# Performance work log

Hardware: AMD Instinct MI355X
Metric: run time of the kernel (lower is better)

Reference implementation:

```python
import jax, jax.numpy as jnp
import numpy as np

LN_EPS = 1e-5

def _layernorm(x, g, b):
    mu = x.mean(-1, keepdims=True)
    var = ((x - mu) ** 2).mean(-1, keepdims=True)
    return (x - mu) * jax.lax.rsqrt(var + LN_EPS) * g + b

def setup_inputs() -> dict:
    key = jax.random.key(0)
    ks = jax.random.split(key, 5)
    B, S, H, V = 1, 1024, 768, 50257
    return {
        "hidden_states": jax.random.normal(ks[0], (B, S, H), jnp.float32),
        "attention_mask": jnp.ones((B, S), jnp.int32),
        "alpha": jnp.float32(0.1),
        "ln_gamma": jnp.ones((H,), jnp.float32),
        "ln_beta": jnp.zeros((H,), jnp.float32),
        "W1": jax.random.normal(ks[1], (H, H), jnp.float32) * 0.02,
        "b1": jnp.zeros((H,), jnp.float32),
        "W2": jax.random.normal(ks[2], (H, H), jnp.float32) * 0.02,
        "b2": jnp.zeros((H,), jnp.float32),
        "lm_head_w": jax.random.normal(ks[3], (V, H), jnp.float32) * 0.02,
        "n_processors": 4,
        "k_steps": 4,
    }

def reference(hidden_states, attention_mask, alpha, ln_gamma, ln_beta,
              W1, b1, W2, b2, lm_head_w, n_processors, k_steps):
    P = int(n_processors)
    K = int(k_steps)
    mask = attention_mask.astype(hidden_states.dtype)[..., None]        # [B,S,1]
    # processor_states: [P,B,S,H] (all initialized to the same hidden state)
    states = jnp.broadcast_to(hidden_states[None], (P,) + hidden_states.shape)
    for _ in range(K):
        # eval mode: dropout=identity, no noise -> mutate == mask multiply
        mut = states * mask                                             # [P,B,S,H]
        if P > 1:
            # mean of other processors = (sum_all - self)/(P-1)
            observe = (mut.sum(0, keepdims=True) - mut) / (P - 1)
        else:
            observe = jnp.zeros_like(mut)
        merged = mut + alpha * observe
        normed = _layernorm(merged, ln_gamma, ln_beta)
        h = jax.nn.gelu(jnp.einsum('pbsh,ih->pbsi', normed, W1) + b1,
                        approximate=False)
        delta = jnp.einsum('pbsi,hi->pbsh', h, W2) + b2
        states = (mut + delta) * mask
    consensus = states.mean(0)                                          # [B,S,H]
    logits = jnp.einsum('bsh,vh->bsv', consensus, lm_head_w)            # [B,S,V]
    processor_logits = jnp.einsum('pbsh,vh->pbsv', states, lm_head_w)   # [P,B,S,V]
    return logits, processor_logits, states
```

## Files before the change

kernel.cpp:

```cpp
#include <hip/hip_runtime.h>
#include <hip/hip_bf16.h>
#include <math.h>

#define S_LEN 1024
#define HDIM  768
#define NPROC 4
#define VOCAB 50257
#define KSTEPS 4

typedef __attribute__((ext_vector_type(4))) float f32x4;
typedef __attribute__((ext_vector_type(8))) short bf16x8;
typedef __attribute__((ext_vector_type(4))) short short4v;

static __device__ __forceinline__ ushort f2bf(float f) {
  union { __hip_bfloat16 b; ushort u; } cv;
  cv.b = __float2bfloat16(f);
  return cv.u;
}

#define GLOAD16(gp, lp) __builtin_amdgcn_global_load_lds( \
    (const __attribute__((address_space(1))) unsigned int*)(gp), \
    (__attribute__((address_space(3))) unsigned int*)(lp), 16, 0, 0)

__global__ __launch_bounds__(256) void prep_weights(
    const float* __restrict__ lmw, const float* __restrict__ W1,
    const float* __restrict__ W2, ushort* __restrict__ lm_bf,
    ushort* __restrict__ w1_bf, ushort* __restrict__ w2_bf,
    const float* __restrict__ hidden, const int* __restrict__ mask,
    const float* __restrict__ alphap, const float* __restrict__ gamma,
    const float* __restrict__ beta, ushort* __restrict__ normed) {
  const int LM4 = VOCAB * HDIM / 4;
  const int W4  = HDIM * HDIM / 4;
  const int LMB = (LM4 + 255) / 256;
  const int WB  = (W4 + 255) / 256;
  const int bid = blockIdx.x;
  const int tid = threadIdx.x;
  __shared__ float rs_[4], rq_[4];
  if (bid < LMB + 2 * WB) {
    const float* in; ushort* out; int n4, i;
    if (bid < LMB)           { in = lmw; out = lm_bf; n4 = LM4; i = bid * 256 + tid; }
    else if (bid < LMB + WB) { in = W1;  out = w1_bf; n4 = W4;  i = (bid - LMB) * 256 + tid; }
    else                     { in = W2;  out = w2_bf; n4 = W4;  i = (bid - LMB - WB) * 256 + tid; }
    if (i >= n4) return;
    f32x4 v = ((const f32x4*)in)[i];
    short4v o;
#pragma unroll
    for (int j = 0; j < 4; j++) o[j] = (short)f2bf(v[j]);
    ((short4v*)out)[i] = o;
  } else {
    const int s = bid - (LMB + 2 * WB);
    const float mk = (float)mask[s];
    const float a1 = 1.0f + alphap[0];
    float merged[3];
    float lsum = 0.f, lsq = 0.f;
#pragma unroll
    for (int e = 0; e < 3; e++) {
      const int h = tid + e * 256;
      float mg = hidden[(size_t)s * HDIM + h] * mk * a1;
      merged[e] = mg;
      lsum += mg;
      lsq += mg * mg;
    }
#pragma unroll
    for (int off = 32; off > 0; off >>= 1) {
      lsum += __shfl_down(lsum, off, 64);
      lsq  += __shfl_down(lsq, off, 64);
    }
    const int wv = tid >> 6, ln = tid & 63;
    if (ln == 0) { rs_[wv] = lsum; rq_[wv] = lsq; }
    __syncthreads();
    const float ts = rs_[0] + rs_[1] + rs_[2] + rs_[3];
    const float tq = rq_[0] + rq_[1] + rq_[2] + rq_[3];
    const float mu = ts * (1.f / HDIM);
    const float var = tq * (1.f / HDIM) - mu * mu;
    const float rstd = rsqrtf(var + 1e-5f);
#pragma unroll
    for (int e = 0; e < 3; e++) {
      const int h = tid + e * 256;
      float nv = (merged[e] - mu) * rstd * gamma[h] + beta[h];
      normed[(size_t)s * HDIM + h] = f2bf(nv);
    }
  }
}

__global__ __launch_bounds__(256) void bcast_logits(
    const float* __restrict__ src, float* __restrict__ dst) {
  const size_t n4 = (size_t)S_LEN * VOCAB / 4;
  for (size_t i = (size_t)blockIdx.x * 256 + threadIdx.x; i < n4;
       i += (size_t)gridDim.x * 256) {
    f32x4 v = ((const f32x4*)src)[i];
#pragma unroll
    for (int p = 0; p < NPROC; p++)
      ((f32x4*)dst)[(size_t)p * n4 + i] = v;
  }
}

__global__ __launch_bounds__(256) void merge_ln_p1(
    const float* __restrict__ src, const int* __restrict__ mask,
    const float* __restrict__ alphap, const float* __restrict__ gamma,
    const float* __restrict__ beta, ushort* __restrict__ normed) {
  const int s = blockIdx.x;
  const int tid = threadIdx.x;
  const float mk = (float)mask[s];
  const float a1 = 1.0f + alphap[0];
  float merged[3];
  float lsum = 0.f, lsq = 0.f;
#pragma unroll
  for (int e = 0; e < 3; e++) {
    const int h = tid + e * 256;
    float mg = src[(size_t)s * HDIM + h] * mk * a1;
    merged[e] = mg;
    lsum += mg;
    lsq += mg * mg;
  }
#pragma unroll
  for (int off = 32; off > 0; off >>= 1) {
    lsum += __shfl_down(lsum, off, 64);
    lsq  += __shfl_down(lsq, off, 64);
  }
  __shared__ float rs_[4], rq_[4];
  const int wv = tid >> 6, ln = tid & 63;
  if (ln == 0) { rs_[wv] = lsum; rq_[wv] = lsq; }
  __syncthreads();
  const float ts = rs_[0] + rs_[1] + rs_[2] + rs_[3];
  const float tq = rq_[0] + rq_[1] + rq_[2] + rq_[3];
  const float mu = ts * (1.f / HDIM);
  const float var = tq * (1.f / HDIM) - mu * mu;
  const float rstd = rsqrtf(var + 1e-5f);
#pragma unroll
  for (int e = 0; e < 3; e++) {
    const int h = tid + e * 256;
    float nv = (merged[e] - mu) * rstd * gamma[h] + beta[h];
    normed[(size_t)s * HDIM + h] = f2bf(nv);
  }
}

template <int MODE>
__global__ __launch_bounds__(256, 4) void gemm_mlp(
    const ushort* __restrict__ A, const ushort* __restrict__ B,
    const float* __restrict__ bias, ushort* __restrict__ out_bf,
    const float* __restrict__ src, float* __restrict__ dst,
    float* __restrict__ states, const int* __restrict__ mask) {
  __shared__ __align__(16) ushort lsA[3][4096];
  __shared__ __align__(16) ushort lsB[3][2048];
  const int tid = threadIdx.x;
  const int bx = blockIdx.x;
  const int mt = bx & 7;
  const int nt = bx >> 3;
  const int wv = tid >> 6, lane = tid & 63;
  const int wm = wv >> 1, wn = wv & 1;
  const int g = lane >> 4, lr = lane & 15;

  f32x4 acc[4][2];
#pragma unroll
  for (int i = 0; i < 4; i++)
#pragma unroll
    for (int j = 0; j < 2; j++) acc[i][j] = (f32x4){0.f, 0.f, 0.f, 0.f};

  const int koff = (tid & 3) * 8;
  const int arow0 = mt * 128 + (tid >> 2);
  const ushort* gA0 = A + (size_t)arow0 * HDIM + koff;
  const ushort* gA1 = gA0 + (size_t)64 * HDIM;
  const ushort* gB0 = B + (size_t)(nt * 64 + (tid >> 2)) * HDIM + koff;
  const int dstl = (tid >> 2) * 32 + (tid & 3) * 8;

#define STAGE(kt, buf) do {                      \
    const int o_ = (kt) * 32;                    \
    GLOAD16(gA0 + o_, &lsA[buf][dstl]);          \
    GLOAD16(gA1 + o_, &lsA[buf][2048 + dstl]);   \
    GLOAD16(gB0 + o_, &lsB[buf][dstl]);          \
  } while (0)

  constexpr int NT = HDIM / 32;
  STAGE(0, 0);
  STAGE(1, 1);
  STAGE(2, 2);
  int cur = 0;
  for (int kt = 0; kt < NT; ++kt) {
    if (kt < NT - 2)      asm volatile("s_waitcnt vmcnt(6)" ::: "memory");
    else if (kt == NT - 2) asm volatile("s_waitcnt vmcnt(3)" ::: "memory");
    else                  asm volatile("s_waitcnt vmcnt(0)" ::: "memory");
    __builtin_amdgcn_s_barrier();
    __builtin_amdgcn_sched_barrier(0);
    bf16x8 af[4], bfr[2];
#pragma unroll
    for (int mi = 0; mi < 4; mi++)
      af[mi] = *(const bf16x8*)(&lsA[cur][(wm * 64 + mi * 16 + lr) * 32 + g * 8]);
#pragma unroll
    for (int ni = 0; ni < 2; ni++)
      bfr[ni] = *(const bf16x8*)(&lsB[cur][(wn * 32 + ni * 16 + lr) * 32 + g * 8]);
    asm volatile("s_waitcnt lgkmcnt(0)" ::: "memory");
    __builtin_amdgcn_sched_barrier(0);
    __builtin_amdgcn_s_setprio(1);
#pragma unroll
    for (int mi = 0; mi < 4; mi++)
#pragma unroll
      for (int ni = 0; ni < 2; ni++)
        acc[mi][ni] = __builtin_amdgcn_mfma_f32_16x16x32_bf16(af[mi], bfr[ni], acc[mi][ni], 0, 0, 0);
    __builtin_amdgcn_s_setprio(0);
    __builtin_amdgcn_s_barrier();
    __builtin_amdgcn_sched_barrier(0);
    if (kt + 3 < NT) STAGE(kt + 3, cur);
    cur = (cur == 2) ? 0 : cur + 1;
  }
#undef STAGE

#pragma unroll
  for (int mi = 0; mi < 4; mi++) {
    const int mrow = mt * 128 + wm * 64 + mi * 16 + g * 4;
#pragma unroll
    for (int ni = 0; ni < 2; ni++) {
      const int ncol = nt * 64 + wn * 32 + ni * 16 + lr;
      const float bv = bias[ncol];
      if (MODE == 0) {
#pragma unroll
        for (int j = 0; j < 4; j++) {
          float x = acc[mi][ni][j] + bv;
          float ge = 0.5f * x * (1.f + erff(x * 0.70710678118654752f));
          out_bf[(size_t)(mrow + j) * HDIM + ncol] = f2bf(ge);
        }
      } else {
#pragma unroll
        for (int j = 0; j < 4; j++) {
          const int m = mrow + j;
          const float mk = (float)mask[m];
          const size_t idx = (size_t)m * HDIM + ncol;
          const float mut = src[idx] * mk;
          const float ns = (mut + acc[mi][ni][j] + bv) * mk;
          if (out_bf) {
            out_bf[idx] = f2bf(ns);
#pragma unroll
            for (int p = 0; p < NPROC; p++)
              states[(size_t)p * S_LEN * HDIM + idx] = ns;
          } else {
            dst[idx] = ns;
          }
        }
      }
    }
  }
}

__global__ __launch_bounds__(512, 2) void gemm_lm(
    const ushort* __restrict__ A, const ushort* __restrict__ B,
    float* __restrict__ logits, int nrowsB) {
  __shared__ __align__(16) ushort lds[2][4][8192];
  ushort* ldsb = &lds[0][0][0];
  const int tid = threadIdx.x;
  const int bx = blockIdx.x;
  const int mt = bx & 3;
  const int nt = bx >> 2;
  const int wv = tid >> 6, lane = tid & 63;
  const int wm = wv >> 2, wn = wv & 3;
  const int g = lane >> 4, lr = lane & 15;

  f32x4 acc[8][4];
#pragma unroll
  for (int i = 0; i < 8; i++)
#pragma unroll
    for (int j = 0; j < 4; j++) acc[i][j] = (f32x4){0.f, 0.f, 0.f, 0.f};

  const ushort* gsrc[4][2];
#pragma unroll
  for (int j = 0; j < 2; j++) {
    const int c = j * 512 + wv * 64 + lane;
    const int qa = c >> 9, ra = (c >> 3) & 63, oa = (c & 7) ^ (ra & 7);
    gsrc[0][j] = A + (size_t)(mt * 256 + qa * 128 + ra) * HDIM + oa * 8;
    gsrc[1][j] = A + (size_t)(mt * 256 + qa * 128 + 64 + ra) * HDIM + oa * 8;
    const int qb = c >> 8, rb = (c >> 3) & 31, ob = (c & 7) ^ (rb & 7);
    int r2 = nt * 256 + qb * 64 + rb;      if (r2 >= nrowsB) r2 = nrowsB - 1;
    int r3 = nt * 256 + qb * 64 + 32 + rb; if (r3 >= nrowsB) r3 = nrowsB - 1;
    gsrc[2][j] = B + (size_t)r2 * HDIM + ob * 8;
    gsrc[3][j] = B + (size_t)r3 * HDIM + ob * 8;
  }
  const int a_lane = wm * 4096 + lr * 64;
  const int b_lane = wn * 2048 + lr * 64;
  int slot8[2];
  slot8[0] = ((0 + g) ^ (lr & 7)) * 8;
  slot8[1] = ((4 + g) ^ (lr & 7)) * 8;

#define STG(R_, tt_) do {                                                     \
    ushort* dst_ = ldsb + (size_t)((((tt_) & 1) * 4 + (R_)) * 8192 + wv * 512); \
    GLOAD16(gsrc[R_][0] + (size_t)(tt_) * 64, dst_);                          \
    GLOAD16(gsrc[R_][1] + (size_t)(tt_) * 64, dst_ + 4096);                   \
  } while (0)

#define MFMA_Q(MB, NB, AV, BV) do {                                           \
    __builtin_amdgcn_s_setprio(1);                                           \
    _Pragma("unroll")                                                        \
    for (int mi = 0; mi < 4; mi++)                                           \
      _Pragma("unroll")                                                      \
      for (int ni = 0; ni < 2; ni++)                                         \
        _Pragma("unroll")                                                    \
        for (int ks = 0; ks < 2; ks++)                                       \
          acc[(MB) + mi][(NB) + ni] = __builtin_amdgcn_mfma_f32_16x16x32_bf16( \
              AV[mi][ks], BV[ni][ks], acc[(MB) + mi][(NB) + ni], 0, 0, 0);   \
    __builtin_amdgcn_s_setprio(0);                                           \
  } while (0)

  constexpr int NT = HDIM / 64;
  STG(0, 0); STG(2, 0); STG(3, 0); STG(1, 0);
  asm volatile("s_waitcnt vmcnt(4)" ::: "memory");
  __builtin_amdgcn_sched_barrier(0);
  __builtin_amdgcn_s_barrier();

  bf16x8 af[4][2], blo[2][2], bhi[2][2];
  for (int t = 0; t < NT - 1; ++t) {
    const ushort* cp = ldsb + (size_t)(t & 1) * 32768;
#pragma unroll
    for (int mi = 0; mi < 4; mi++)
#pragma unroll
      for (int ks = 0; ks < 2; ks++)
        af[mi][ks] = *(const bf16x8*)(cp + a_lane + mi * 1024 + slot8[ks]);
#pragma unroll
    for (int ni = 0; ni < 2; ni++)
#pragma unroll
      for (int ks = 0; ks < 2; ks++)
        blo[ni][ks] = *(const bf16x8*)(cp + 16384 + b_lane + ni * 1024 + slot8[ks]);
    STG(0, t + 1);
    __builtin_amdgcn_s_barrier();
    asm volatile("s_waitcnt lgkmcnt(0)" ::: "memory");
    __builtin_amdgcn_sched_barrier(0);
    MFMA_Q(0, 0, af, blo);
    asm volatile("s_waitcnt vmcnt(4)" ::: "memory");
    __builtin_amdgcn_sched_barrier(0);
    __builtin_amdgcn_s_barrier();
#pragma unroll
    for (int ni = 0; ni < 2; ni++)
#pragma unroll
      for (int ks = 0; ks < 2; ks++)
        bhi[ni][ks] = *(const bf16x8*)(cp + 24576 + b_lane + ni * 1024 + slot8[ks]);
    STG(2, t + 1);
    __builtin_amdgcn_s_barrier();
    asm volatile("s_waitcnt lgkmcnt(0)" ::: "memory");
    __builtin_amdgcn_sched_barrier(0);
    MFMA_Q(0, 2, af, bhi);
    asm volatile("s_waitcnt vmcnt(4)" ::: "memory");
    __builtin_amdgcn_sched_barrier(0);
    __builtin_amdgcn_s_barrier();
#pragma unroll
    for (int mi = 0; mi < 4; mi++)
#pragma unroll
      for (int ks = 0; ks < 2; ks++)
        af[mi][ks] = *(const bf16x8*)(cp + 8192 + a_lane + mi * 1024 + slot8[ks]);
    STG(3, t + 1);
    __builtin_amdgcn_s_barrier();
    asm volatile("s_waitcnt lgkmcnt(0)" ::: "memory");
    __builtin_amdgcn_sched_barrier(0);
    MFMA_Q(4, 2, af, bhi);
    __builtin_amdgcn_s_barrier();
    STG(1, t + 1);
    __builtin_amdgcn_s_barrier();
    MFMA_Q(4, 0, af, blo);
    asm volatile("s_waitcnt vmcnt(4)" ::: "memory");
    __builtin_amdgcn_sched_barrier(0);
    __builtin_amdgcn_s_barrier();
  }
  {
    const int t = NT - 1;
    const ushort* cp = ldsb + (size_t)(t & 1) * 32768;
#pragma unroll
    for (int mi = 0; mi < 4; mi++)
#pragma unroll
      for (int ks = 0; ks < 2; ks++)
        af[mi][ks] = *(const bf16x8*)(cp + a_lane + mi * 1024 + slot8[ks]);
#pragma unroll
    for (int ni = 0; ni < 2; ni++)
#pragma unroll
      for (int ks = 0; ks < 2; ks++)
        blo[ni][ks] = *(const bf16x8*)(cp + 16384 + b_lane + ni * 1024 + slot8[ks]);
    __builtin_amdgcn_s_barrier();
    asm volatile("s_waitcnt lgkmcnt(0)" ::: "memory");
    __builtin_amdgcn_sched_barrier(0);
    MFMA_Q(0, 0, af, blo);
    asm volatile("s_waitcnt vmcnt(2)" ::: "memory");
    __builtin_amdgcn_sched_barrier(0);
    __builtin_amdgcn_s_barrier();
#pragma unroll
    for (int ni = 0; ni < 2; ni++)
#pragma unroll
      for (int ks = 0; ks < 2; ks++)
        bhi[ni][ks] = *(const bf16x8*)(cp + 24576 + b_lane + ni * 1024 + slot8[ks]);
    __builtin_amdgcn_s_barrier();
    asm volatile("s_waitcnt lgkmcnt(0)" ::: "memory");
    __builtin_amdgcn_sched_barrier(0);
    MFMA_Q(0, 2, af, bhi);
    asm volatile("s_waitcnt vmcnt(0)" ::: "memory");
    __builtin_amdgcn_sched_barrier(0);
    __builtin_amdgcn_s_barrier();
#pragma unroll
    for (int mi = 0; mi < 4; mi++)
#pragma unroll
      for (int ks = 0; ks < 2; ks++)
        af[mi][ks] = *(const bf16x8*)(cp + 8192 + a_lane + mi * 1024 + slot8[ks]);
    asm volatile("s_waitcnt lgkmcnt(0)" ::: "memory");
    __builtin_amdgcn_sched_barrier(0);
    MFMA_Q(4, 2, af, bhi);
    MFMA_Q(4, 0, af, blo);
  }
#undef STG
#undef MFMA_Q

  float* sc = ((float*)ldsb) + wv * 1024;
  const int cbase = nt * 256 + wn * 64 + lane;
  const bool cok = cbase < nrowsB;
#pragma unroll
  for (int mi = 0; mi < 8; mi++) {
    __syncthreads();
#pragma unroll
    for (int ni = 0; ni < 4; ni++)
#pragma unroll
      for (int j = 0; j < 4; j++)
        sc[(g * 4 + j) * 64 + ni * 16 + lr] = acc[mi][ni][j];
    __syncthreads();
    const int srow0 = mt * 256 + wm * 128 + mi * 16;
    if (cok) {
#pragma unroll
      for (int r = 0; r < 16; r++)
        logits[(size_t)(srow0 + r) * VOCAB + cbase] = sc[r * 64 + lane];
    }
  }
}

extern "C" void kernel_launch(void* const* d_in, const int* in_sizes, int n_in,
                              void* d_out, int out_size, void* d_ws, size_t ws_size,
                              hipStream_t stream) {
  const float* hidden = (const float*)d_in[0];
  const int*   mask   = (const int*)d_in[1];
  const float* alphap = (const float*)d_in[2];
  const float* gamma  = (const float*)d_in[3];
  const float* beta   = (const float*)d_in[4];
  const float* W1     = (const float*)d_in[5];
  const float* b1     = (const float*)d_in[6];
  const float* W2     = (const float*)d_in[7];
  const float* b2     = (const float*)d_in[8];
  const float* lmw    = (const float*)d_in[9];

  float* logits  = (float*)d_out;
  float* plogits = logits + (size_t)S_LEN * VOCAB;
  float* states  = plogits + (size_t)NPROC * S_LEN * VOCAB;

  uint8_t* ws = (uint8_t*)d_ws;
  ushort* lm_bf  = (ushort*)ws;
  ushort* w1_bf  = (ushort*)(ws + 77194752);
  ushort* w2_bf  = (ushort*)(ws + 78374400);
  ushort* nrm_bf = (ushort*)(ws + 79554048);
  ushort* h_bf   = (ushort*)(ws + 81126912);
  ushort* a_bf   = (ushort*)(ws + 82699776);
  float*  st1    = (float*) (ws + 84272640);
  if (ws_size < 87418368) return;

  const int LMB = (VOCAB * HDIM / 4 + 255) / 256, WB = (HDIM * HDIM / 4 + 255) / 256;
  prep_weights<<<LMB + 2 * WB + S_LEN, 256, 0, stream>>>(
      lmw, W1, W2, lm_bf, w1_bf, w2_bf, hidden, mask, alphap, gamma, beta, nrm_bf);

  for (int k = 0; k < KSTEPS; k++) {
    const float* src = (k == 0) ? hidden : st1;
    if (k > 0)
      merge_ln_p1<<<S_LEN, 256, 0, stream>>>(src, mask, alphap, gamma, beta, nrm_bf);
    gemm_mlp<0><<<(HDIM / 64) * 8, 256, 0, stream>>>(
        nrm_bf, w1_bf, b1, h_bf, nullptr, nullptr, nullptr, mask);
    gemm_mlp<1><<<(HDIM / 64) * 8, 256, 0, stream>>>(
        h_bf, w2_bf, b2, (k == KSTEPS - 1) ? (ushort*)a_bf : nullptr,
        src, st1, states, mask);
  }
  gemm_lm<<<((VOCAB + 255) / 256) * 4, 512, 0, stream>>>(a_bf, lm_bf, logits, VOCAB);
  bcast_logits<<<2048, 256, 0, stream>>>(logits, plogits);
}
```

Measured before the change: 542.0 us.

## Make LM-head GEMM persistent with resident A slice and streamed B tiles

Rewrites the vocab projection GEMM as a persistent 256-block kernel. Each block keeps its 64-row activation slice resident in LDS and loops over a contiguous range of 128-column weight tiles, pipelining 32-wide K chunks through a 4-slot ring. Results are written directly from registers instead of through an LDS staging pass. This removes repeated A loads and the epilogue shuffle, but uses smaller tiles, one block per CU, and relies on L2 to absorb repeated weight reads across the 16 row groups.

```diff
diff --git a/kernel.cpp b/kernel.cpp
--- a/kernel.cpp
+++ b/kernel.cpp
@@ -241,185 +241,105 @@
   }
 }
 
-__global__ __launch_bounds__(512, 2) void gemm_lm(
+__global__ __launch_bounds__(256, 1) void gemm_lm(
     const ushort* __restrict__ A, const ushort* __restrict__ B,
-    float* __restrict__ logits, int nrowsB) {
-  __shared__ __align__(16) ushort lds[2][4][8192];
-  ushort* ldsb = &lds[0][0][0];
+    float* __restrict__ logits) {
+  __shared__ __align__(16) ushort lsA[49152];
+  __shared__ __align__(16) ushort lsB[4][4096];
   const int tid = threadIdx.x;
   const int bx = blockIdx.x;
-  const int mt = bx & 3;
-  const int nt = bx >> 2;
+  const int m0 = (bx & 15) * 64;
+  const int grp = bx >> 4;
+  constexpr int NTILES = (VOCAB + 127) / 128;
+  constexpr int QCH = (NTILES + 15) / 16;
+  const int nt0 = grp * QCH;
+  const int nt1 = (nt0 + QCH < NTILES) ? nt0 + QCH : NTILES;
   const int wv = tid >> 6, lane = tid & 63;
-  const int wm = wv >> 2, wn = wv & 3;
+  const int wm = wv >> 1, wn = wv & 1;
   const int g = lane >> 4, lr = lane & 15;
 
-  f32x4 acc[8][4];
-#pragma unroll
-  for (int i = 0; i < 8; i++)
+#pragma unroll
+  for (int r = 0; r < 24; r++) {
+    const int c = r * 256 + wv * 64 + lane;
+    const int kt = c >> 8, cc = c & 255, row = cc >> 2, p = cc & 3;
+    const int s = p ^ (row & 3);
+    GLOAD16(A + (size_t)(m0 + row) * HDIM + kt * 32 + s * 8,
+            lsA + (size_t)(r * 256 + wv * 64) * 8);
+  }
+
+#define STGB(ntv, tv, sl) do {                                            \
+    _Pragma("unroll")                                                     \
+    for (int jj = 0; jj < 2; jj++) {                                      \
+      const int c_ = jj * 256 + wv * 64 + lane;                           \
+      const int row_ = c_ >> 2, p_ = c_ & 3;                              \
+      const int s_ = p_ ^ (row_ & 3);                                     \
+      int rg_ = (ntv) * 128 + row_; if (rg_ >= VOCAB) rg_ = VOCAB - 1;    \
+      GLOAD16(B + (size_t)rg_ * HDIM + (tv) * 32 + s_ * 8,                \
+              &lsB[sl][(size_t)(jj * 256 + wv * 64) * 8]);                \
+    }                                                                     \
+  } while (0)
+
+  STGB(nt0, 0, 0); STGB(nt0, 1, 1); STGB(nt0, 2, 2);
+
+  f32x4 acc[2][4];
+#pragma unroll
+  for (int i = 0; i < 2; i++)
 #pragma unroll
     for (int j = 0; j < 4; j++) acc[i][j] = (f32x4){0.f, 0.f, 0.f, 0.f};
 
-  const ushort* gsrc[4][2];
-#pragma unroll
-  for (int j = 0; j < 2; j++) {
-    const int c = j * 512 + wv * 64 + lane;
-    const int qa = c >> 9, ra = (c >> 3) & 63, oa = (c & 7) ^ (ra & 7);
-    gsrc[0][j] = A + (size_t)(mt * 256 + qa * 128 + ra) * HDIM + oa * 8;
-    gsrc[1][j] = A + (size_t)(mt * 256 + qa * 128 + 64 + ra) * HDIM + oa * 8;
-    const int qb = c >> 8, rb = (c >> 3) & 31, ob = (c & 7) ^ (rb & 7);
-    int r2 = nt * 256 + qb * 64 + rb;      if (r2 >= nrowsB) r2 = nrowsB - 1;
-    int r3 = nt * 256 + qb * 64 + 32 + rb; if (r3 >= nrowsB) r3 = nrowsB - 1;
-    gsrc[2][j] = B + (size_t)r2 * HDIM + ob * 8;
-    gsrc[3][j] = B + (size_t)r3 * HDIM + ob * 8;
-  }
-  const int a_lane = wm * 4096 + lr * 64;
-  const int b_lane = wn * 2048 + lr * 64;
-  int slot8[2];
-  slot8[0] = ((0 + g) ^ (lr & 7)) * 8;
-  slot8[1] = ((4 + g) ^ (lr & 7)) * 8;
-
-#define STG(R_, tt_) do {                                                     \
-    ushort* dst_ = ldsb + (size_t)((((tt_) & 1) * 4 + (R_)) * 8192 + wv * 512); \
-    GLOAD16(gsrc[R_][0] + (size_t)(tt_) * 64, dst_);                          \
-    GLOAD16(gsrc[R_][1] + (size_t)(tt_) * 64, dst_ + 4096);                   \
-  } while (0)
-
-#define MFMA_Q(MB, NB, AV, BV) do {                                           \
-    __builtin_amdgcn_s_setprio(1);                                           \
-    _Pragma("unroll")                                                        \
-    for (int mi = 0; mi < 4; mi++)                                           \
-      _Pragma("unroll")                                                      \
-      for (int ni = 0; ni < 2; ni++)                                         \
-        _Pragma("unroll")                                                    \
-        for (int ks = 0; ks < 2; ks++)                                       \
-          acc[(MB) + mi][(NB) + ni] = __builtin_amdgcn_mfma_f32_16x16x32_bf16( \
-              AV[mi][ks], BV[ni][ks], acc[(MB) + mi][(NB) + ni], 0, 0, 0);   \
-    __builtin_amdgcn_s_setprio(0);                                           \
-  } while (0)
-
-  constexpr int NT = HDIM / 64;
-  STG(0, 0); STG(2, 0); STG(3, 0); STG(1, 0);
-  asm volatile("s_waitcnt vmcnt(4)" ::: "memory");
-  __builtin_amdgcn_sched_barrier(0);
-  __builtin_amdgcn_s_barrier();
-
-  bf16x8 af[4][2], blo[2][2], bhi[2][2];
-  for (int t = 0; t < NT - 1; ++t) {
-    const ushort* cp = ldsb + (size_t)(t & 1) * 32768;
-#pragma unroll
-    for (int mi = 0; mi < 4; mi++)
-#pragma unroll
-      for (int ks = 0; ks < 2; ks++)
-        af[mi][ks] = *(const bf16x8*)(cp + a_lane + mi * 1024 + slot8[ks]);
-#pragma unroll
-    for (int ni = 0; ni < 2; ni++)
-#pragma unroll
-      for (int ks = 0; ks < 2; ks++)
-        blo[ni][ks] = *(const bf16x8*)(cp + 16384 + b_lane + ni * 1024 + slot8[ks]);
-    STG(0, t + 1);
+  const int xslot = ((lr & 3)) << 3;
+  constexpr int NKT = HDIM / 32;
+
+  for (int nt = nt0; nt < nt1; ++nt) {
+    for (int t = 0; t < NKT; ++t) {
+      if (t < NKT - 2)       asm volatile("s_waitcnt vmcnt(4)" ::: "memory");
+      else if (t == NKT - 2) asm volatile("s_waitcnt vmcnt(2)" ::: "memory");
+      else                   asm volatile("s_waitcnt vmcnt(0)" ::: "memory");
+      __builtin_amdgcn_sched_barrier(0);
+      __builtin_amdgcn_s_barrier();
+      __builtin_amdgcn_sched_barrier(0);
+      const int sl = t & 3;
+      bf16x8 af[2], bfr[4];
+#pragma unroll
+      for (int mi = 0; mi < 2; mi++)
+        af[mi] = *(const bf16x8*)(lsA + t * 2048 + (wm * 32 + mi * 16 + lr) * 32 +
+                                  ((g << 3) ^ xslot));
+#pragma unroll
+      for (int ni = 0; ni < 4; ni++)
+        bfr[ni] = *(const bf16x8*)(&lsB[sl][(wn * 64 + ni * 16 + lr) * 32 +
+                                            ((g << 3) ^ xslot)]);
+      asm volatile("s_waitcnt lgkmcnt(0)" ::: "memory");
+      __builtin_amdgcn_sched_barrier(0);
+      __builtin_amdgcn_s_setprio(1);
+#pragma unroll
+      for (int mi = 0; mi < 2; mi++)
+#pragma unroll
+        for (int ni = 0; ni < 4; ni++)
+          acc[mi][ni] = __builtin_amdgcn_mfma_f32_16x16x32_bf16(af[mi], bfr[ni], acc[mi][ni], 0, 0, 0);
+      __builtin_amdgcn_s_setprio(0);
+      __builtin_amdgcn_s_barrier();
+      __builtin_amdgcn_sched_barrier(0);
+      if (t + 3 < NKT) STGB(nt, t + 3, (t + 3) & 3);
+    }
     __builtin_amdgcn_s_barrier();
-    asm volatile("s_waitcnt lgkmcnt(0)" ::: "memory");
-    __builtin_amdgcn_sched_barrier(0);
-    MFMA_Q(0, 0, af, blo);
-    asm volatile("s_waitcnt vmcnt(4)" ::: "memory");
-    __builtin_amdgcn_sched_barrier(0);
-    __builtin_amdgcn_s_barrier();
-#pragma unroll
-    for (int ni = 0; ni < 2; ni++)
-#pragma unroll
-      for (int ks = 0; ks < 2; ks++)
-        bhi[ni][ks] = *(const bf16x8*)(cp + 24576 + b_lane + ni * 1024 + slot8[ks]);
-    STG(2, t + 1);
-    __builtin_amdgcn_s_barrier();
-    asm volatile("s_waitcnt lgkmcnt(0)" ::: "memory");
-    __builtin_amdgcn_sched_barrier(0);
-    MFMA_Q(0, 2, af, bhi);
-    asm volatile("s_waitcnt vmcnt(4)" ::: "memory");
-    __builtin_amdgcn_sched_barrier(0);
-    __builtin_amdgcn_s_barrier();
-#pragma unroll
-    for (int mi = 0; mi < 4; mi++)
-#pragma unroll
-      for (int ks = 0; ks < 2; ks++)
-        af[mi][ks] = *(const bf16x8*)(cp + 8192 + a_lane + mi * 1024 + slot8[ks]);
-    STG(3, t + 1);
-    __builtin_amdgcn_s_barrier();
-    asm volatile("s_waitcnt lgkmcnt(0)" ::: "memory");
-    __builtin_amdgcn_sched_barrier(0);
-    MFMA_Q(4, 2, af, bhi);
-    __builtin_amdgcn_s_barrier();
-    STG(1, t + 1);
-    __builtin_amdgcn_s_barrier();
-    MFMA_Q(4, 0, af, blo);
-    asm volatile("s_waitcnt vmcnt(4)" ::: "memory");
-    __builtin_amdgcn_sched_barrier(0);
-    __builtin_amdgcn_s_barrier();
-  }
-  {
-    const int t = NT - 1;
-    const ushort* cp = ldsb + (size_t)(t & 1) * 32768;
-#pragma unroll
-    for (int mi = 0; mi < 4; mi++)
-#pragma unroll
-      for (int ks = 0; ks < 2; ks++)
-        af[mi][ks] = *(const bf16x8*)(cp + a_lane + mi * 1024 + slot8[ks]);
-#pragma unroll
-    for (int ni = 0; ni < 2; ni++)
-#pragma unroll
-      for (int ks = 0; ks < 2; ks++)
-        blo[ni][ks] = *(const bf16x8*)(cp + 16384 + b_lane + ni * 1024 + slot8[ks]);
-    __builtin_amdgcn_s_barrier();
-    asm volatile("s_waitcnt lgkmcnt(0)" ::: "memory");
-    __builtin_amdgcn_sched_barrier(0);
-    MFMA_Q(0, 0, af, blo);
-    asm volatile("s_waitcnt vmcnt(2)" ::: "memory");
-    __builtin_amdgcn_sched_barrier(0);
-    __builtin_amdgcn_s_barrier();
-#pragma unroll
-    for (int ni = 0; ni < 2; ni++)
-#pragma unroll
-      for (int ks = 0; ks < 2; ks++)
-        bhi[ni][ks] = *(const bf16x8*)(cp + 24576 + b_lane + ni * 1024 + slot8[ks]);
-    __builtin_amdgcn_s_barrier();
-    asm volatile("s_waitcnt lgkmcnt(0)" ::: "memory");
-    __builtin_amdgcn_sched_barrier(0);
-    MFMA_Q(0, 2, af, bhi);
-    asm volatile("s_waitcnt vmcnt(0)" ::: "memory");
-    __builtin_amdgcn_sched_barrier(0);
-    __builtin_amdgcn_s_barrier();
-#pragma unroll
-    for (int mi = 0; mi < 4; mi++)
-#pragma unroll
-      for (int ks = 0; ks < 2; ks++)
-        af[mi][ks] = *(const bf16x8*)(cp + 8192 + a_lane + mi * 1024 + slot8[ks]);
-    asm volatile("s_waitcnt lgkmcnt(0)" ::: "memory");
-    __builtin_amdgcn_sched_barrier(0);
-    MFMA_Q(4, 2, af, bhi);
-    MFMA_Q(4, 0, af, blo);
-  }
-#undef STG
-#undef MFMA_Q
-
-  float* sc = ((float*)ldsb) + wv * 1024;
-  const int cbase = nt * 256 + wn * 64 + lane;
-  const bool cok = cbase < nrowsB;
-#pragma unroll
-  for (int mi = 0; mi < 8; mi++) {
-    __syncthreads();
-#pragma unroll
-    for (int ni = 0; ni < 4; ni++)
-#pragma unroll
-      for (int j = 0; j < 4; j++)
-        sc[(g * 4 + j) * 64 + ni * 16 + lr] = acc[mi][ni][j];
-    __syncthreads();
-    const int srow0 = mt * 256 + wm * 128 + mi * 16;
-    if (cok) {
-#pragma unroll
-      for (int r = 0; r < 16; r++)
-        logits[(size_t)(srow0 + r) * VOCAB + cbase] = sc[r * 64 + lane];
-    }
-  }
+    if (nt + 1 < nt1) { STGB(nt + 1, 0, 0); STGB(nt + 1, 1, 1); STGB(nt + 1, 2, 2); }
+    const int n0 = nt * 128;
+#pragma unroll
+    for (int mi = 0; mi < 2; mi++) {
+      const int row0 = m0 + wm * 32 + mi * 16 + g * 4;
+#pragma unroll
+      for (int ni = 0; ni < 4; ni++) {
+        const int col = n0 + wn * 64 + ni * 16 + lr;
+        if (col < VOCAB) {
+#pragma unroll
+          for (int j = 0; j < 4; j++)
+            logits[(size_t)(row0 + j) * VOCAB + col] = acc[mi][ni][j];
+        }
+        acc[mi][ni] = (f32x4){0.f, 0.f, 0.f, 0.f};
+      }
+    }
+  }
+#undef STGB
 }
 
 extern "C" void kernel_launch(void* const* d_in, const int* in_sizes, int n_in,
@@ -464,6 +384,6 @@
         h_bf, w2_bf, b2, (k == KSTEPS - 1) ? (ushort*)a_bf : nullptr,
         src, st1, states, mask);
   }
-  gemm_lm<<<((VOCAB + 255) / 256) * 4, 512, 0, stream>>>(a_bf, lm_bf, logits, VOCAB);
+  gemm_lm<<<256, 256, 0, stream>>>(a_bf, lm_bf, logits);
   bcast_logits<<<2048, 256, 0, stream>>>(logits, plogits);
 }
```

Result: slower. 774.1 us (+42.8%).
